# Optimization experiments

Hardware: AMD Instinct MI355X
Metric: run time of the kernel (lower is better)

## Reference

```python
import jax, jax.numpy as jnp
import numpy as np

NH = 8          # num_heads
EMB = 256       # embed_dim
HD = EMB // NH  # head_dim
NV = 6          # num_views
NL = 4          # num_fmap_levels
NP = 4          # num_ref_points
NZ = 4          # num_z_ref_points
OFFSET_SCALE = 1.0
SHAPES = [(64, 64), (32, 32), (16, 16), (8, 8)]
SLEN = sum(h * w for h, w in SHAPES)  # 5440


def setup_inputs() -> dict:
    key = jax.random.key(0)
    ks = jax.random.split(key, 9)
    N, Q = 1, 1600
    A = NH * NV * NL * NP * NZ  # total sampling slots per query
    s = 0.02
    return {
        "queries": jax.random.normal(ks[0], (N, Q, EMB), jnp.float32),
        # pre-normalized reference points in [-1, 1] (normalize_ref_points=False path)
        "ref_points": jax.random.uniform(ks[1], (N, Q, NV, NL, NZ, 2), jnp.float32, -1.0, 1.0),
        "value": jax.random.normal(ks[2], (N, NV, SLEN, EMB), jnp.float32),
        "value_spatial_shapes": jnp.asarray(SHAPES, jnp.int32),
        "Wv": jax.random.normal(ks[3], (EMB, EMB), jnp.float32) * s,
        "Woff": jax.random.normal(ks[4], (A * 2, EMB), jnp.float32) * s,
        "boff": jnp.zeros((A * 2,), jnp.float32),
        "Wattn": jax.random.normal(ks[5], (A, EMB), jnp.float32) * s,
        "battn": jnp.zeros((A,), jnp.float32),
        "Wout": jax.random.normal(ks[6], (EMB, EMB), jnp.float32) * s,
    }


def _forward(queries, ref_points, value, shapes_np, Wv, Woff, boff, Wattn, battn, Wout):
    N, Q, C = queries.shape
    # sampling offsets: tanh-bounded, scaled
    offs = jnp.tanh(queries @ Woff.T + boff) * OFFSET_SCALE
    offs = offs.reshape(N, Q, NH, NV, NL, NP, NZ, 2)
    # attention weights: softmax over all (view, level, point, z) slots per head
    attn = (queries @ Wattn.T + battn).reshape(N, Q, NH, NV * NL * NP * NZ)
    attn = jax.nn.softmax(attn, axis=-1).reshape(N, Q, NH, NV, NL, NP, NZ)
    # value projection, split heads: (N, V, H, S, hd)
    val = (value @ Wv.T).reshape(N, NV, -1, NH, HD)
    val = jnp.transpose(val, (0, 1, 3, 2, 4))
    # sampling locations, clamped to [-1, 1] (grid_sample normalized coords)
    locs = jnp.clip(ref_points[:, :, None, :, :, None, :, :] + offs, -1.0, 1.0)  # (N,Q,H,V,L,P,Z,2)
    locs = jnp.transpose(locs, (0, 3, 2, 4, 1, 5, 6, 7))   # (N,V,H,L,Q,P,Z,2)
    attn_t = jnp.transpose(attn, (0, 3, 2, 4, 1, 5, 6))     # (N,V,H,L,Q,P,Z)

    out = jnp.zeros((N, Q, NH, HD), queries.dtype)
    start = 0
    for l in range(NL):
        Hl, Wl = int(shapes_np[l, 0]), int(shapes_np[l, 1])
        S = Hl * Wl
        fmap = val[:, :, :, start:start + S, :]  # (N,V,H,S,hd)
        g = locs[:, :, :, l].reshape(N, NV, NH, Q * NP * NZ, 2)
        # align_corners=True mapping; coords are clamped so zero-padding never triggers
        x = (g[..., 0] + 1.0) * 0.5 * (Wl - 1)
        y = (g[..., 1] + 1.0) * 0.5 * (Hl - 1)
        x0 = jnp.floor(x); y0 = jnp.floor(y)
        wx = x - x0; wy = y - y0
        x0i = jnp.clip(x0.astype(jnp.int32), 0, Wl - 1)
        y0i = jnp.clip(y0.astype(jnp.int32), 0, Hl - 1)
        x1i = jnp.clip(x0i + 1, 0, Wl - 1)
        y1i = jnp.clip(y0i + 1, 0, Hl - 1)

        def gat(yi, xi):
            return jnp.take_along_axis(fmap, (yi * Wl + xi)[..., None], axis=3)

        samp = (((1 - wy) * (1 - wx))[..., None] * gat(y0i, x0i)
                + ((1 - wy) * wx)[..., None] * gat(y0i, x1i)
                + (wy * (1 - wx))[..., None] * gat(y1i, x0i)
                + (wy * wx)[..., None] * gat(y1i, x1i))  # (N,V,H,QPZ,hd)
        samp = samp.reshape(N, NV, NH, Q, NP, NZ, HD)
        out = out + jnp.einsum('nvhqpzd,nvhqpz->nqhd', samp, attn_t[:, :, :, l])
        start += S

    out = out.reshape(N, Q, C)
    return out @ Wout.T  # out_fc (dropout is identity at inference)


def reference(queries, ref_points, value, value_spatial_shapes, Wv, Woff, boff, Wattn, battn, Wout):
    shapes_np = np.asarray(value_spatial_shapes)
    return _forward(queries, ref_points, value, shapes_np, Wv, Woff, boff, Wattn, battn, Wout)
```

## Files before the change

kernel.cpp:

```cpp
#include <hip/hip_runtime.h>
#include <hip/hip_bf16.h>
#include <math.h>

#define NHh   8
#define EMB   256
#define HDd   32
#define NVv   6
#define SLENs 5440
#define QQ    1600
#define A_ATTN 3072
#define A_OFF  6144

typedef _Float16 half8 __attribute__((ext_vector_type(8)));
typedef __attribute__((ext_vector_type(4))) float f32x4;

__device__ __forceinline__ unsigned short f2bf(float f) {
  __hip_bfloat16 h = __float2bfloat16(f);
  return *(unsigned short*)&h;
}
__device__ __forceinline__ unsigned short f2h(float f) {
  _Float16 h = (_Float16)f;
  return __builtin_bit_cast(unsigned short, h);
}
__device__ __forceinline__ float h2f(unsigned short u) {
  return (float)__builtin_bit_cast(_Float16, u);
}

__device__ __forceinline__ void dma16(const unsigned short* g, unsigned short* l) {
  __builtin_amdgcn_global_load_lds(
      (const __attribute__((address_space(1))) unsigned int*)g,
      (__attribute__((address_space(3))) unsigned int*)l, 16, 0, 0);
}

__global__ __launch_bounds__(256) void split_h_kernel(
    const float* __restrict__ q, const float* __restrict__ value,
    const float* __restrict__ Woff, const float* __restrict__ Wattn,
    const float* __restrict__ Wv, const float* __restrict__ Wout,
    unsigned short* __restrict__ q16, unsigned short* __restrict__ v16,
    unsigned short* __restrict__ Wq16, unsigned short* __restrict__ Wv16,
    unsigned short* __restrict__ Wout16) {
  int i4 = blockIdx.x * 256 + threadIdx.x;
  const float* src; unsigned short* dst; int sloc; int dloc;
  if      (i4 < 102400)  { src = q;     dst = q16;    sloc = i4;           dloc = sloc; }
  else if (i4 < 2191360) { src = value; dst = v16;    sloc = i4 - 102400;  dloc = sloc; }
  else if (i4 < 2584576) { src = Woff;  dst = Wq16;   sloc = i4 - 2191360; dloc = sloc; }
  else if (i4 < 2781184) { src = Wattn; dst = Wq16;   sloc = i4 - 2584576; dloc = sloc + 393216; }
  else if (i4 < 2797568) { src = Wv;    dst = Wv16;   sloc = i4 - 2781184; dloc = sloc; }
  else                   { src = Wout;  dst = Wout16; sloc = i4 - 2797568; dloc = sloc; }
  float4 x = ((const float4*)src)[sloc];
  ushort4 hh;
  hh.x = f2h(x.x); hh.y = f2h(x.y); hh.z = f2h(x.z); hh.w = f2h(x.w);
  ((ushort4*)dst)[dloc] = hh;
}

__global__ __launch_bounds__(256) void gemm23_kernel(
    const unsigned short* __restrict__ q16, const unsigned short* __restrict__ Wq16,
    const unsigned short* __restrict__ v16, const unsigned short* __restrict__ Wv16,
    const float* __restrict__ boff, const float* __restrict__ battn,
    unsigned short* __restrict__ offs16, unsigned short* __restrict__ attn16,
    unsigned short* __restrict__ val_t) {
  __shared__ unsigned short LAh[128 * 32], LBh[128 * 32];

  const int bid = blockIdx.x;
  const unsigned short *A, *B;
  int M, bm, bn;
  bool isVal;
  if (bid < 936) {
    A = q16;  B = Wq16;  M = QQ;
    bn = (bid % 72) * 128;  bm = (bid / 72) * 128;  isVal = false;
  } else {
    int b2 = bid - 936;
    A = v16;  B = Wv16;  M = NVv * SLENs;
    bn = (b2 & 1) * 128;  bm = (b2 >> 1) * 128;  isVal = true;
  }
  const int K = EMB;

  const int tid = threadIdx.x;
  const int lane = tid & 63, w = tid >> 6;
  const int wm = (w & 1) * 64, wn = (w >> 1) * 64;
  const int l16 = lane & 15, quad = lane >> 4;

  const int c0 = tid, c1 = tid + 256;
  const int r0 = c0 >> 2, s0 = (c0 & 3) * 8;
  const int r1 = c1 >> 2, s1 = (c1 & 3) * 8;
  const size_t a0 = (size_t)min(bm + r0, M - 1) * K + s0;
  const size_t a1 = (size_t)min(bm + r1, M - 1) * K + s1;
  const size_t b0o = (size_t)(bn + r0) * K + s0;
  const size_t b1o = (size_t)(bn + r1) * K + s1;
  const int l0 = c0 * 8, l1 = c1 * 8;

  f32x4 acc[4][4] = {};

  for (int k0 = 0; k0 < K; k0 += 32) {
    dma16(&A[a0 + k0], &LAh[l0]);
    dma16(&A[a1 + k0], &LAh[l1]);
    dma16(&B[b0o + k0], &LBh[l0]);
    dma16(&B[b1o + k0], &LBh[l1]);
    __syncthreads();

    half8 fa[4], fb[4];
#pragma unroll
    for (int i = 0; i < 4; ++i) {
      int ar = (wm + i * 16 + l16) * 32 + quad * 8;
      int br = (wn + i * 16 + l16) * 32 + quad * 8;
      fa[i] = *(const half8*)&LAh[ar];
      fb[i] = *(const half8*)&LBh[br];
    }
#pragma unroll
    for (int i = 0; i < 4; ++i)
#pragma unroll
      for (int j = 0; j < 4; ++j)
        acc[i][j] = __builtin_amdgcn_mfma_f32_16x16x32_f16(fa[i], fb[j], acc[i][j], 0, 0, 0);
    __syncthreads();
  }

#pragma unroll
  for (int j = 0; j < 4; ++j) {
    int n = bn + wn + j * 16 + l16;
    float bv = 0.f;
    bool dotanh = false;
    if (!isVal) {
      if (n < A_OFF) { bv = boff[n]; dotanh = true; }
      else bv = battn[n - A_OFF];
    }
#pragma unroll
    for (int i = 0; i < 4; ++i) {
      int mbase = bm + wm + i * 16 + quad * 4;
#pragma unroll
      for (int reg = 0; reg < 4; ++reg) {
        int m = mbase + reg;
        if (m >= M) continue;
        float c = acc[i][j][reg] + bv;
        if (isVal) {
          int vv = m / SLENs;
          int s = m - vv * SLENs;
          int hh2 = n >> 5, dd = n & 31;
          val_t[((size_t)(vv * 8 + hh2) * SLENs + s) * 32 + dd] = f2h(c);
        } else if (dotanh) {
          float t = __expf(2.f * c);
          c = 1.f - 2.f / (t + 1.f);
          offs16[(size_t)m * A_OFF + n] = f2h(c);
        } else {
          attn16[(size_t)m * A_ATTN + (n - A_OFF)] = f2h(c);
        }
      }
    }
  }
}

__global__ __launch_bounds__(256) void gemmh0_kernel(
    const unsigned short* __restrict__ Ah, const unsigned short* __restrict__ Bh,
    float* __restrict__ C, int M, int N, int K) {
  __shared__ unsigned short LAh[128 * 32], LBh[128 * 32];

  const int tid = threadIdx.x;
  const int bm = blockIdx.y * 128, bn = blockIdx.x * 128;
  const int lane = tid & 63, w = tid >> 6;
  const int wm = (w & 1) * 64, wn = (w >> 1) * 64;
  const int l16 = lane & 15, quad = lane >> 4;

  const int c0 = tid, c1 = tid + 256;
  const int r0 = c0 >> 2, s0 = (c0 & 3) * 8;
  const int r1 = c1 >> 2, s1 = (c1 & 3) * 8;
  const size_t a0 = (size_t)min(bm + r0, M - 1) * K + s0;
  const size_t a1 = (size_t)min(bm + r1, M - 1) * K + s1;
  const size_t b0o = (size_t)(bn + r0) * K + s0;
  const size_t b1o = (size_t)(bn + r1) * K + s1;
  const int l0 = c0 * 8, l1 = c1 * 8;

  f32x4 acc[4][4] = {};

  for (int k0 = 0; k0 < K; k0 += 32) {
    dma16(&Ah[a0 + k0], &LAh[l0]);
    dma16(&Ah[a1 + k0], &LAh[l1]);
    dma16(&Bh[b0o + k0], &LBh[l0]);
    dma16(&Bh[b1o + k0], &LBh[l1]);
    __syncthreads();

    half8 fa[4], fb[4];
#pragma unroll
    for (int i = 0; i < 4; ++i) {
      int ar = (wm + i * 16 + l16) * 32 + quad * 8;
      int br = (wn + i * 16 + l16) * 32 + quad * 8;
      fa[i] = *(const half8*)&LAh[ar];
      fb[i] = *(const half8*)&LBh[br];
    }
#pragma unroll
    for (int i = 0; i < 4; ++i)
#pragma unroll
      for (int j = 0; j < 4; ++j)
        acc[i][j] = __builtin_amdgcn_mfma_f32_16x16x32_f16(fa[i], fb[j], acc[i][j], 0, 0, 0);
    __syncthreads();
  }

#pragma unroll
  for (int j = 0; j < 4; ++j) {
    int n = bn + wn + j * 16 + l16;
#pragma unroll
    for (int i = 0; i < 4; ++i) {
      int mbase = bm + wm + i * 16 + quad * 4;
#pragma unroll
      for (int reg = 0; reg < 4; ++reg) {
        int m = mbase + reg;
        if (m >= M) continue;
        C[(size_t)m * N + n] = acc[i][j][reg];
      }
    }
  }
}

__global__ __launch_bounds__(256) void sample_kernel(
    const float* __restrict__ ref, const unsigned short* __restrict__ offs16,
    const unsigned short* __restrict__ attn16,
    const unsigned short* __restrict__ val_t,
    unsigned short* __restrict__ op16) {
  __shared__ int4 Lrec[4][384];

  const int h   = blockIdx.x & 7;
  const int qt  = blockIdx.x >> 3;
  const int wid = threadIdx.x >> 6;
  const int lane = threadIdx.x & 63;
  const int q   = qt * 4 + wid;
  const int row = q * 8 + h;

  {
    const unsigned short* ap = attn16 + (size_t)row * 384;
    float vals[6];
    float mx = -1e30f;
#pragma unroll
    for (int i = 0; i < 6; ++i) { vals[i] = h2f(ap[lane + i * 64]); mx = fmaxf(mx, vals[i]); }
#pragma unroll
    for (int o = 32; o > 0; o >>= 1) mx = fmaxf(mx, __shfl_xor(mx, o, 64));
    float s = 0.f;
#pragma unroll
    for (int i = 0; i < 6; ++i) { vals[i] = __expf(vals[i] - mx); s += vals[i]; }
#pragma unroll
    for (int o = 32; o > 0; o >>= 1) s += __shfl_xor(s, o, 64);
    const float inv = 1.0f / s;

    const int l = (lane >> 4) & 3;
    const int z = lane & 3;
    const int Wl = 64 >> l;
    const int start = (l == 0) ? 0 : (l == 1 ? 4096 : (l == 2 ? 5120 : 5376));
    const float sc = 0.5f * (float)(Wl - 1);
    const unsigned int* op = (const unsigned int*)offs16 + (size_t)row * 384;
    const float* rq = ref + (size_t)q * (NVv * 4 * 4 * 2);

#pragma unroll 1
    for (int v = 0; v < 6; ++v) {
      int j = v * 64 + lane;
      float w = vals[v] * inv;
      unsigned int oxy = op[j];
      float ox = h2f((unsigned short)(oxy & 0xFFFF));
      float oy = h2f((unsigned short)(oxy >> 16));
      const float* rp = rq + ((v * 4 + l) * 4 + z) * 2;
      float rx = rp[0], ry = rp[1];
      float x = fminf(1.f, fmaxf(-1.f, rx + ox));
      float y = fminf(1.f, fmaxf(-1.f, ry + oy));
      float xp = (x + 1.f) * sc, yp = (y + 1.f) * sc;
      float x0f = floorf(xp), y0f = floorf(yp);
      int x0 = (int)x0f, y0 = (int)y0f;
      float wx = xp - x0f, wy = yp - y0f;
      int i00 = start + y0 * Wl + x0;
      int dxe = (x0 + 1 < Wl) ? 1 : 0;
      int dye = (y0 + 1 < Wl) ? Wl : 0;
      int i10 = i00 + dye;
      float wxw = wx * w, wmx = w - wxw;
      float w01 = wxw * (1.f - wy), w11 = wxw * wy;
      float w00 = wmx * (1.f - wy), w10 = wmx * wy;
      Lrec[wid][j] = make_int4(
          i00 | ((i00 + dxe) << 16),
          i10 | ((i10 + dxe) << 16),
          (int)(((unsigned)f2h(w01) << 16) | f2h(w00)),
          (int)(((unsigned)f2h(w11) << 16) | f2h(w10)));
    }
  }

  const int cb    = (lane >> 2) & 3;
  const int e16   = (lane & 3) << 4;
  const int r     = lane >> 4;
  const int sel   = cb >> 1;
  const int shamt = (cb & 1) << 4;

  const unsigned* Lw = (const unsigned*)&Lrec[wid][0];

  float acc[8] = {};

#pragma unroll 1
  for (int v = 0; v < 6; ++v) {
    const char* sb = (const char*)val_t + (size_t)(v * 8 + h) * (SLENs * 64);
    const int rbase = v * 64 + r;
#pragma unroll 4
    for (int t = 0; t < 16; ++t) {
      int ri = rbase + t * 4;
      unsigned iw = Lw[ri * 4 + sel];
      unsigned wb = Lw[ri * 4 + 2 + sel];
      int off = (int)((iw >> shamt) & 0xFFFFu) << 6;
      float wl_ = (float)__builtin_bit_cast(_Float16, (unsigned short)(wb >> shamt));
      uint4 u = *(const uint4*)(sb + (off + e16));
      half8 vh = __builtin_bit_cast(half8, u);
#pragma unroll
      for (int c = 0; c < 8; ++c)
        acc[c] = fmaf(wl_, (float)vh[c], acc[c]);
    }
  }

#pragma unroll
  for (int m = 4; m <= 32; m <<= 1)
#pragma unroll
    for (int j = 0; j < 8; ++j) acc[j] += __shfl_xor(acc[j], m, 64);

  if (lane < 4) {
    int off = q * EMB + h * 32 + lane * 8;
    ushort4 h0, h1;
    h0.x = f2h(acc[0]); h0.y = f2h(acc[1]); h0.z = f2h(acc[2]); h0.w = f2h(acc[3]);
    h1.x = f2h(acc[4]); h1.y = f2h(acc[5]); h1.z = f2h(acc[6]); h1.w = f2h(acc[7]);
    *(ushort4*)&op16[off] = h0;  *(ushort4*)&op16[off + 4] = h1;
  }
}

extern "C" void kernel_launch(void* const* d_in, const int* in_sizes, int n_in,
                              void* d_out, int out_size, void* d_ws, size_t ws_size,
                              hipStream_t stream) {
  const float* queries    = (const float*)d_in[0];
  const float* ref_points = (const float*)d_in[1];
  const float* value      = (const float*)d_in[2];
  const float* Wv    = (const float*)d_in[4];
  const float* Woff  = (const float*)d_in[5];
  const float* boff  = (const float*)d_in[6];
  const float* Wattn = (const float*)d_in[7];
  const float* battn = (const float*)d_in[8];
  const float* Wout  = (const float*)d_in[9];
  float* out = (float*)d_out;

  char* W = (char*)d_ws;
  unsigned short* offs16 = (unsigned short*)(W + 0);
  unsigned short* attn16 = (unsigned short*)(W + 19660800);
  unsigned short* val_t  = (unsigned short*)(W + 29491200);
  unsigned short* q16    = (unsigned short*)(W + 46202880);
  unsigned short* v16    = (unsigned short*)(W + 47022080);
  unsigned short* Wq16   = (unsigned short*)(W + 63733760);
  unsigned short* Wv16   = (unsigned short*)(W + 68452352);
  unsigned short* Wout16 = (unsigned short*)(W + 68583424);
  unsigned short* op16   = (unsigned short*)(W + 68714496);

  dim3 blk(256);

  split_h_kernel<<<10992, blk, 0, stream>>>(
      queries, value, Woff, Wattn, Wv, Wout, q16, v16, Wq16, Wv16, Wout16);
  gemm23_kernel<<<1446, blk, 0, stream>>>(
      q16, Wq16, v16, Wv16, boff, battn, offs16, attn16, val_t);
  sample_kernel<<<QQ * NHh / 4, blk, 0, stream>>>(
      ref_points, offs16, attn16, val_t, op16);
  gemmh0_kernel<<<dim3(EMB / 128, (QQ + 127) / 128), blk, 0, stream>>>(
      op16, Wout16, out, QQ, EMB, EMB);
}
```

Before: 209.4 us.

## Pack index and weight per corner, swizzle GEMM tiles, unroll gather loop more

Packs each bilinear corner's 16-bit index and fp16 weight into one 32-bit word, so a gather lane issues a single LDS read instead of two reads plus shifts and selects. Remaps GEMM block IDs so consecutive blocks share the same M tile across groups of N tiles, aiming at better L2 reuse. Raises the inner gather loop unroll from 4 to 8 to get more loads in flight, which may increase register pressure.

New measurement: 205.3 us. No clear change (-2.0%).

```diff
diff --git a/kernel.cpp b/kernel.cpp
--- a/kernel.cpp
+++ b/kernel.cpp
@@ -66,8 +66,10 @@
   int M, bm, bn;
   bool isVal;
   if (bid < 936) {
+    int x = bid & 7, i = bid >> 3;
+    int nt = x * 9 + (i % 9), mt = i / 9;
     A = q16;  B = Wq16;  M = QQ;
-    bn = (bid % 72) * 128;  bm = (bid / 72) * 128;  isVal = false;
+    bn = nt * 128;  bm = mt * 128;  isVal = false;
   } else {
     int b2 = bid - 936;
     A = v16;  B = Wv16;  M = NVv * SLENs;
@@ -261,26 +263,24 @@
       float x0f = floorf(xp), y0f = floorf(yp);
       int x0 = (int)x0f, y0 = (int)y0f;
       float wx = xp - x0f, wy = yp - y0f;
-      int i00 = start + y0 * Wl + x0;
-      int dxe = (x0 + 1 < Wl) ? 1 : 0;
-      int dye = (y0 + 1 < Wl) ? Wl : 0;
-      int i10 = i00 + dye;
+      unsigned i00 = (unsigned)(start + y0 * Wl + x0);
+      unsigned dxe = (x0 + 1 < Wl) ? 1u : 0u;
+      unsigned dye = (y0 + 1 < Wl) ? (unsigned)Wl : 0u;
+      unsigned i10 = i00 + dye;
       float wxw = wx * w, wmx = w - wxw;
       float w01 = wxw * (1.f - wy), w11 = wxw * wy;
       float w00 = wmx * (1.f - wy), w10 = wmx * wy;
       Lrec[wid][j] = make_int4(
-          i00 | ((i00 + dxe) << 16),
-          i10 | ((i10 + dxe) << 16),
-          (int)(((unsigned)f2h(w01) << 16) | f2h(w00)),
-          (int)(((unsigned)f2h(w11) << 16) | f2h(w10)));
-    }
-  }
-
-  const int cb    = (lane >> 2) & 3;
-  const int e16   = (lane & 3) << 4;
-  const int r     = lane >> 4;
-  const int sel   = cb >> 1;
-  const int shamt = (cb & 1) << 4;
+          (int)(i00         | ((unsigned)f2h(w00) << 16)),
+          (int)((i00 + dxe) | ((unsigned)f2h(w01) << 16)),
+          (int)(i10         | ((unsigned)f2h(w10) << 16)),
+          (int)((i10 + dxe) | ((unsigned)f2h(w11) << 16)));
+    }
+  }
+
+  const int cb  = (lane >> 2) & 3;
+  const int e16 = (lane & 3) << 4;
+  const int r   = lane >> 4;
 
   const unsigned* Lw = (const unsigned*)&Lrec[wid][0];
 
@@ -290,15 +290,14 @@
   for (int v = 0; v < 6; ++v) {
     const char* sb = (const char*)val_t + (size_t)(v * 8 + h) * (SLENs * 64);
     const int rbase = v * 64 + r;
-#pragma unroll 4
+#pragma unroll 8
     for (int t = 0; t < 16; ++t) {
       int ri = rbase + t * 4;
-      unsigned iw = Lw[ri * 4 + sel];
-      unsigned wb = Lw[ri * 4 + 2 + sel];
-      int off = (int)((iw >> shamt) & 0xFFFFu) << 6;
-      float wl_ = (float)__builtin_bit_cast(_Float16, (unsigned short)(wb >> shamt));
-      uint4 u = *(const uint4*)(sb + (off + e16));
-      half8 vh = __builtin_bit_cast(half8, u);
+      unsigned u = Lw[ri * 4 + cb];
+      int off = (int)(u & 0xFFFFu) << 6;
+      float wl_ = (float)__builtin_bit_cast(_Float16, (unsigned short)(u >> 16));
+      uint4 d = *(const uint4*)(sb + (off + e16));
+      half8 vh = __builtin_bit_cast(half8, d);
 #pragma unroll
       for (int c = 0; c < 8; ++c)
         acc[c] = fmaf(wl_, (float)vh[c], acc[c]);
```
